# Kernel optimization log

Hardware: AMD Instinct MI355X
Metric: run time of the kernel (lower is better)

Reference implementation:

```python
import jax, jax.numpy as jnp
import numpy as np

B, H, W, C = 1, 180, 360, 192
WS, SHIFT, NH = 6, 3, 6
MLAT, MLON = H // WS, W // WS
NW = MLAT * MLON
N = WS * WS
HD = C // NH
SCALE = HD ** -0.5
EPS = 1e-5


def _rel_index():
    # earth-specific relative position index: (MLAT, N, N) int32
    ch = np.arange(WS)
    cw = np.arange(WS)
    coords = np.stack(np.meshgrid(ch, cw, indexing='ij')).reshape(2, -1)  # (2, N)
    rel = coords[:, :, None] - coords[:, None, :]                         # (2, N, N)
    idx = (rel[0] + WS - 1) * (2 * WS - 1) + (rel[1] + WS - 1)            # (N, N)
    off = np.arange(MLAT) * (2 * WS - 1) * (2 * WS - 1)                   # per-latitude offset
    return (idx[None, :, :] + off[:, None, None]).astype(np.int32)


def _attn_mask():
    # standard shifted-window mask: (NW, N, N), 0 or -100
    img = np.zeros((H, W), dtype=np.int32)
    cnt = 0
    for hs in (slice(0, -WS), slice(-WS, -SHIFT), slice(-SHIFT, None)):
        for ws_ in (slice(0, -WS), slice(-WS, -SHIFT), slice(-SHIFT, None)):
            img[hs, ws_] = cnt
            cnt += 1
    wins = img.reshape(MLAT, WS, MLON, WS).transpose(0, 2, 1, 3).reshape(NW, N)
    diff = wins[:, None, :] - wins[:, :, None]
    return np.where(diff != 0, -100.0, 0.0).astype(np.float32)

_RPI = jnp.asarray(_rel_index())     # (MLAT, N, N)
_MASK = jnp.asarray(_attn_mask())    # (NW, N, N)


def _layernorm(x, g, b):
    mu = jnp.mean(x, axis=-1, keepdims=True)
    var = jnp.mean(jnp.square(x - mu), axis=-1, keepdims=True)
    return (x - mu) * jax.lax.rsqrt(var + EPS) * g + b


def _window_partition(x):
    # (B, H, W, C) -> (B*NW, N, C)
    x = x.reshape(B, MLAT, WS, MLON, WS, C).transpose(0, 1, 3, 2, 4, 5)
    return x.reshape(B * NW, N, C)


def _window_reverse(w):
    # (B*NW, N, C) -> (B, H, W, C)
    x = w.reshape(B, MLAT, MLON, WS, WS, C).transpose(0, 1, 3, 2, 4, 5)
    return x.reshape(B, H, W, C)


def setup_inputs() -> dict:
    key = jax.random.key(0)
    ks = jax.random.split(key, 6)
    s = 0.02
    return {
        'x': jax.random.normal(ks[0], (B, H * W, C), jnp.float32),
        'norm1_w': jnp.ones((C,), jnp.float32),
        'norm1_b': jnp.zeros((C,), jnp.float32),
        'qkv_w': jax.random.normal(ks[1], (C, 3 * C), jnp.float32) * s,
        'qkv_b': jnp.zeros((3 * C,), jnp.float32),
        'proj_w': jax.random.normal(ks[2], (C, C), jnp.float32) * s,
        'proj_b': jnp.zeros((C,), jnp.float32),
        'bias_table': jax.random.normal(ks[3], (MLAT * (2 * WS - 1) ** 2, NH), jnp.float32) * s,
        'norm2_w': jnp.ones((C,), jnp.float32),
        'norm2_b': jnp.zeros((C,), jnp.float32),
        'fc1_w': jax.random.normal(ks[4], (C, 4 * C), jnp.float32) * s,
        'fc1_b': jnp.zeros((4 * C,), jnp.float32),
        'fc2_w': jax.random.normal(ks[5], (4 * C, C), jnp.float32) * s,
        'fc2_b': jnp.zeros((C,), jnp.float32),
    }


def reference(x, norm1_w, norm1_b, qkv_w, qkv_b, proj_w, proj_b, bias_table,
              norm2_w, norm2_b, fc1_w, fc1_b, fc2_w, fc2_b):
    shortcut = x
    h = _layernorm(x, norm1_w, norm1_b).reshape(B, H, W, C)
    # cyclic shift
    h = jnp.roll(h, shift=(-SHIFT, -SHIFT), axis=(1, 2))
    xw = _window_partition(h)                                   # (B*NW, N, C)

    qkv = xw @ qkv_w + qkv_b                                    # (B_, N, 3C)
    qkv = qkv.reshape(B * NW, N, 3, NH, HD).transpose(2, 0, 3, 1, 4)
    q, k, v = qkv[0], qkv[1], qkv[2]                            # (B_, NH, N, HD)

    # earth-specific relative position bias, gathered per latitude row
    bias = jnp.take(bias_table, _RPI, axis=0)                   # (MLAT, N, N, NH)
    bias = bias.transpose(0, 3, 1, 2)[:, None]                  # (MLAT, 1, NH, N, N)
    bias = jnp.broadcast_to(bias, (MLAT, MLON, NH, N, N)).reshape(NW, NH, N, N)
    bias = bias + _MASK[:, None]                                # add shift mask

    attn = jnp.einsum('bhnd,bhmd->bhnm', q, k) * SCALE + bias
    attn = jax.nn.softmax(attn, axis=-1)
    av = jnp.einsum('bhnm,bhmd->bhnd', attn, v)                 # (B_, NH, N, HD)
    av = av.transpose(0, 2, 1, 3).reshape(B * NW, N, C)
    av = av @ proj_w + proj_b

    h = _window_reverse(av)
    h = jnp.roll(h, shift=(SHIFT, SHIFT), axis=(1, 2)).reshape(B, H * W, C)
    x = shortcut + h

    m = _layernorm(x, norm2_w, norm2_b)
    m = jax.nn.gelu(m @ fc1_w + fc1_b, approximate=False) @ fc2_w + fc2_b
    return x + m
```

## Files before the change

kernel.cpp:

```cpp
#include <hip/hip_runtime.h>
#include <hip/hip_bf16.h>

constexpr int HH   = 180;
constexpr int WW   = 360;
constexpr int CC   = 192;
constexpr int WS   = 6;
constexpr int SHIFT= 3;
constexpr int NH   = 6;
constexpr int MLAT = HH / WS;
constexpr int MLON = WW / WS;
constexpr int NWIN = MLAT * MLON;
constexpr int NTOK = WS * WS;
constexpr int HD   = CC / NH;
constexpr long M_TOK = (long)NWIN * NTOK;
constexpr long M_PAD = 65024;
constexpr float SCALE_F = 0.17677669529663687f;

typedef unsigned short ushort_t;
using bf16x8 = __attribute__((ext_vector_type(8))) short;
using f32x4  = __attribute__((ext_vector_type(4))) float;

static __device__ inline float b2f(ushort_t u) {
    union { float f; unsigned int i; } v; v.i = ((unsigned int)u) << 16; return v.f;
}
static __device__ inline ushort_t f2b(float f) {
    __hip_bfloat16 h = __float2bfloat16(f);
    return *(ushort_t*)&h;
}
static __device__ inline unsigned int cvtpk(float lo, float hi) {
    unsigned int r;
    asm("v_cvt_pk_bf16_f32 %0, %1, %2" : "=v"(r) : "v"(lo), "v"(hi));
    return r;
}

static __device__ inline void gload_lds16(const ushort_t* g, ushort_t* l) {
    __builtin_amdgcn_global_load_lds(
        (const __attribute__((address_space(1))) unsigned int*)g,
        (__attribute__((address_space(3))) unsigned int*)l, 16, 0, 0);
}

static __device__ inline int win_map(int ti) {
    int w = ti / NTOK, n = ti - w * NTOK;
    int mlat = w / MLON, mlon = w - mlat * MLON;
    int sh = mlat * WS + n / WS, sw = mlon * WS + (n % WS);
    int hh = sh + SHIFT; if (hh >= HH) hh -= HH;
    int ww2 = sw + SHIFT; if (ww2 >= WW) ww2 -= WW;
    return hh * WW + ww2;
}

__global__ void transpose_all(const float* __restrict__ qkv_w, const float* __restrict__ proj_w,
                              const float* __restrict__ fc1_w, const float* __restrict__ fc2_w,
                              ushort_t* __restrict__ wqkv, ushort_t* __restrict__ wproj,
                              ushort_t* __restrict__ wfc1, ushort_t* __restrict__ wfc2) {
    int e = blockIdx.x * 256 + threadIdx.x;
    const float* in; ushort_t* out; int K, N;
    if (e < 110592)      { in = qkv_w;  out = wqkv;  K = 192; N = 576; }
    else if (e < 147456) { e -= 110592; in = proj_w; out = wproj; K = 192; N = 192; }
    else if (e < 294912) { e -= 147456; in = fc1_w;  out = wfc1;  K = 192; N = 768; }
    else if (e < 442368) { e -= 294912; in = fc2_w;  out = wfc2;  K = 768; N = 192; }
    else return;
    int n = e / K, k = e - n * K;
    out[e] = f2b(in[(long)k * N + n]);
}

__global__ void zero_bf16(ushort_t* __restrict__ p, int count) {
    int e = blockIdx.x * 256 + threadIdx.x;
    if (e < count) p[e] = 0;
}

static __device__ inline int region1d(int p, int L) {
    return (p < L - WS) ? 0 : ((p < L - SHIFT) ? 1 : 2);
}

__global__ void bias_mask_precompute(const float* __restrict__ bt, float* __restrict__ bm) {
    int idx = blockIdx.x * 256 + threadIdx.x;
    if (idx >= MLAT * 2 * NH * 36 * 48) return;
    int e = idx;
    int j = e % 48; e /= 48;
    int i = e % 36; e /= 36;
    int h = e % NH; e /= NH;
    int lt = e % 2;
    int mlat = e / 2;
    if (j >= 36) { bm[idx] = -1e30f; return; }
    int ih = i / WS, iw = i - ih * WS;
    int jh = j / WS, jw = j - jh * WS;
    int bidx = mlat * 121 + (ih - jh + 5) * 11 + (iw - jw + 5);
    float v = bt[bidx * NH + h];
    int mlon = lt ? (MLON - 1) : 0;
    int ri = region1d(mlat * WS + ih, HH) * 3 + region1d(mlon * WS + iw, WW);
    int rj = region1d(mlat * WS + jh, HH) * 3 + region1d(mlon * WS + jw, WW);
    if (ri != rj) v += -100.0f;
    bm[idx] = v;
}

__global__ __launch_bounds__(256) void ln1_window_kernel(
    const float* __restrict__ x, const float* __restrict__ g, const float* __restrict__ b,
    ushort_t* __restrict__ xw)
{
    long t = (long)blockIdx.x * 4 + (threadIdx.x >> 6);
    int lane = threadIdx.x & 63;
    if (t >= M_PAD) return;
    if (t >= M_TOK) {
        ushort_t* o = xw + t * CC;
        o[lane] = 0; o[lane + 64] = 0; o[lane + 128] = 0;
        return;
    }
    int pp = win_map((int)t);
    const float* row = x + (long)pp * CC;
    float v0 = row[lane], v1 = row[lane + 64], v2 = row[lane + 128];
    float s = v0 + v1 + v2;
    float ss = v0 * v0 + v1 * v1 + v2 * v2;
    #pragma unroll
    for (int o = 32; o > 0; o >>= 1) { s += __shfl_xor(s, o, 64); ss += __shfl_xor(ss, o, 64); }
    float mu = s * (1.0f / CC);
    float var = ss * (1.0f / CC) - mu * mu;
    float rinv = rsqrtf(var + 1e-5f);
    ushort_t* o = xw + t * CC;
    o[lane]       = f2b((v0 - mu) * rinv * g[lane]       + b[lane]);
    o[lane + 64]  = f2b((v1 - mu) * rinv * g[lane + 64]  + b[lane + 64]);
    o[lane + 128] = f2b((v2 - mu) * rinv * g[lane + 128] + b[lane + 128]);
}

#define BM 128
#define BN 192
#define BK 64

template<int MODE, int KK>
__global__ __launch_bounds__(512, 4) void gemm_bf16(
    const ushort_t* __restrict__ A, const ushort_t* __restrict__ Bt,
    const float* __restrict__ bias,
    ushort_t* __restrict__ outb, float* __restrict__ outf,
    const float* __restrict__ resid,
    const float* __restrict__ g2, const float* __restrict__ b2,
    int N, long Mguard, int ncol, int nwg)
{
    constexpr int nt = KK / BK;
    __shared__ __align__(16) ushort_t lds[40960];

    int tid = threadIdx.x;
    int lane = tid & 63;
    int wid = tid >> 6;
    int lr = lane & 15, lg = lane >> 4;
    int wm = wid >> 2, wn = wid & 3;

    int orig = blockIdx.x;
    int q = nwg >> 3, r8 = nwg & 7;
    int xcd = orig & 7, pos = orig >> 3;
    int wg = (xcd < r8 ? xcd * (q + 1) : r8 * (q + 1) + (xcd - r8) * q) + pos;
    int brow = wg / ncol, bcol = wg - brow * ncol;
    long bm0 = (long)brow * BM;
    int n0 = bcol * BN;

#define STAGE(b, k0) do { \
    char* base = (char*)lds + (b) * 40960; \
    _Pragma("unroll") \
    for (int i = 0; i < 5; ++i) { \
        int abs_b = tid * 16 + i * 8192; \
        int isA = abs_b < 16384; \
        int loc = isA ? abs_b : abs_b - 16384; \
        int row = loc >> 7, cb = loc & 127; \
        int scol = (cb ^ ((row & 7) << 4)) >> 1; \
        const ushort_t* src = isA ? &A[(bm0 + row) * KK + (k0) + scol] \
                                  : &Bt[(long)(n0 + row) * KK + (k0) + scol]; \
        gload_lds16(src, (ushort_t*)(base + abs_b)); \
    } \
} while (0)

    f32x4 acc[4][3] = {};

    STAGE(0, 0);
    asm volatile("s_waitcnt vmcnt(0)" ::: "memory");
    __builtin_amdgcn_s_barrier();

    int xr = (lr & 7) << 4;

    #pragma unroll
    for (int kt = 0; kt < nt; ++kt) {
        if (kt + 1 < nt) {
            STAGE((kt + 1) & 1, (kt + 1) * BK);
            asm volatile("s_waitcnt vmcnt(5)" ::: "memory");
        } else {
            asm volatile("s_waitcnt vmcnt(0)" ::: "memory");
        }
        __builtin_amdgcn_s_barrier();

        const char* base = (const char*)lds + (kt & 1) * 40960;
        __builtin_amdgcn_s_setprio(1);
        #pragma unroll
        for (int s = 0; s < 2; ++s) {
            bf16x8 af[4], bfr[3];
            #pragma unroll
            for (int fm = 0; fm < 4; ++fm) {
                int row = wm * 64 + fm * 16 + lr;
                af[fm] = *(const bf16x8*)(base + row * 128 + ((s * 64 + lg * 16) ^ xr));
            }
            #pragma unroll
            for (int fn = 0; fn < 3; ++fn) {
                int row = wn * 48 + fn * 16 + lr;
                bfr[fn] = *(const bf16x8*)(base + 16384 + row * 128 + ((s * 64 + lg * 16) ^ xr));
            }
            #pragma unroll
            for (int fm = 0; fm < 4; ++fm)
                #pragma unroll
                for (int fn = 0; fn < 3; ++fn)
                    acc[fm][fn] = __builtin_amdgcn_mfma_f32_16x16x32_bf16(af[fm], bfr[fn], acc[fm][fn], 0, 0, 0);
        }
        __builtin_amdgcn_s_setprio(0);
        asm volatile("s_waitcnt lgkmcnt(0)" ::: "memory");
        __builtin_amdgcn_s_barrier();
    }
#undef STAGE

    float bv[3];
    #pragma unroll
    for (int fn = 0; fn < 3; ++fn) bv[fn] = bias[n0 + wn * 48 + fn * 16 + lr];

    if (MODE == 0 || MODE == 1) {
        ushort_t* bb = lds + wid * 896;
        #pragma unroll
        for (int fm = 0; fm < 4; ++fm) {
            #pragma unroll
            for (int fn = 0; fn < 3; ++fn) {
                #pragma unroll
                for (int r = 0; r < 4; ++r) {
                    float v = acc[fm][fn][r] + bv[fn];
                    if (MODE == 0) {
                        if (n0 == 0) v *= SCALE_F;
                    }
                    if (MODE == 1) {
                        float e2 = exp2f(v * -2.4556617f);
                        v = v * __builtin_amdgcn_rcpf(1.0f + e2);
                    }
                    bb[(lg * 4 + r) * 56 + fn * 16 + lr] = f2b(v);
                }
            }
            #pragma unroll
            for (int i = 0; i < 2; ++i) {
                int cid = i * 64 + lane;
                if (cid < 96) {
                    int row = cid / 6, c6 = cid - row * 6;
                    uint4 val = *(const uint4*)&bb[row * 56 + c6 * 8];
                    long grow = bm0 + wm * 64 + fm * 16 + row;
                    *(uint4*)&outb[grow * (long)N + n0 + wn * 48 + c6 * 8] = val;
                }
            }
        }
    } else if (MODE == 3) {
        float* fb = (float*)lds + wid * 832;
        #pragma unroll
        for (int fm = 0; fm < 4; ++fm) {
            #pragma unroll
            for (int fn = 0; fn < 3; ++fn)
                #pragma unroll
                for (int r = 0; r < 4; ++r)
                    fb[(lg * 4 + r) * 52 + fn * 16 + lr] = acc[fm][fn][r] + bv[fn];
            #pragma unroll
            for (int i = 0; i < 3; ++i) {
                int cid = i * 64 + lane;
                int row = cid / 12, c4 = cid - row * 12;
                f32x4 val = *(const f32x4*)&fb[row * 52 + c4 * 4];
                long grow = bm0 + wm * 64 + fm * 16 + row;
                int col = wn * 48 + c4 * 4;
                if (grow < Mguard) {
                    float* p = &outf[grow * 192 + col];
                    f32x4 old = *(const f32x4*)p;
                    *(f32x4*)p = old + val;
                }
            }
        }
    } else {
        float* redS = (float*)((char*)lds + 73728);
        float* redQ = (float*)((char*)lds + 75776);
        int*   row_map = (int*)((char*)lds + 78336);
        if (tid < BM) {
            long t = bm0 + tid;
            row_map[tid] = (t < M_TOK) ? win_map((int)t) : -1;
        }
        asm volatile("s_waitcnt lgkmcnt(0)" ::: "memory");
        __builtin_amdgcn_s_barrier();

        #pragma unroll
        for (int fm = 0; fm < 4; ++fm) {
            float s4[4], q4[4];
            #pragma unroll
            for (int r = 0; r < 4; ++r) {
                int lrow = wm * 64 + fm * 16 + lg * 4 + r;
                int pp = row_map[lrow];
                float s = 0.f, qq = 0.f;
                #pragma unroll
                for (int fn = 0; fn < 3; ++fn) {
                    float vv = acc[fm][fn][r] + bv[fn];
                    if (pp >= 0) vv += resid[(long)pp * 192 + wn * 48 + fn * 16 + lr];
                    acc[fm][fn][r] = vv;
                    s += vv; qq += vv * vv;
                }
                s4[r] = s; q4[r] = qq;
            }
            #pragma unroll
            for (int off = 1; off < 16; off <<= 1)
                #pragma unroll
                for (int r = 0; r < 4; ++r) {
                    s4[r] += __shfl_xor(s4[r], off, 64);
                    q4[r] += __shfl_xor(q4[r], off, 64);
                }
            if (lr == 0) {
                #pragma unroll
                for (int r = 0; r < 4; ++r) {
                    int row = wm * 64 + fm * 16 + lg * 4 + r;
                    redS[row * 4 + wn] = s4[r];
                    redQ[row * 4 + wn] = q4[r];
                }
            }
        }
        asm volatile("s_waitcnt lgkmcnt(0)" ::: "memory");
        __builtin_amdgcn_s_barrier();

        float gv[3], bv2[3];
        #pragma unroll
        for (int fn = 0; fn < 3; ++fn) {
            gv[fn]  = g2[wn * 48 + fn * 16 + lr];
            bv2[fn] = b2[wn * 48 + fn * 16 + lr];
        }

        float* fb = (float*)lds + wid * 832;
        ushort_t* bb = (ushort_t*)((char*)lds + 32768) + wid * 896;
        #pragma unroll
        for (int fm = 0; fm < 4; ++fm) {
            float mu4[4], rin4[4];
            #pragma unroll
            for (int r = 0; r < 4; ++r) {
                int row = wm * 64 + fm * 16 + lg * 4 + r;
                float s = redS[row * 4 + 0] + redS[row * 4 + 1] + redS[row * 4 + 2] + redS[row * 4 + 3];
                float qq = redQ[row * 4 + 0] + redQ[row * 4 + 1] + redQ[row * 4 + 2] + redQ[row * 4 + 3];
                float mu = s * (1.0f / 192.0f);
                float var = qq * (1.0f / 192.0f) - mu * mu;
                mu4[r] = mu;
                rin4[r] = rsqrtf(var + 1e-5f);
            }
            #pragma unroll
            for (int fn = 0; fn < 3; ++fn)
                #pragma unroll
                for (int r = 0; r < 4; ++r) {
                    float vv = acc[fm][fn][r];
                    fb[(lg * 4 + r) * 52 + fn * 16 + lr] = vv;
                    bb[(lg * 4 + r) * 56 + fn * 16 + lr] =
                        f2b((vv - mu4[r]) * rin4[r] * gv[fn] + bv2[fn]);
                }
            #pragma unroll
            for (int i = 0; i < 3; ++i) {
                int cid = i * 64 + lane;
                int row = cid / 12, c4 = cid - row * 12;
                int pp = row_map[wm * 64 + fm * 16 + row];
                if (pp >= 0) {
                    f32x4 val = *(const f32x4*)&fb[row * 52 + c4 * 4];
                    *(f32x4*)&outf[(long)pp * 192 + wn * 48 + c4 * 4] = val;
                }
            }
            #pragma unroll
            for (int i = 0; i < 2; ++i) {
                int cid = i * 64 + lane;
                if (cid < 96) {
                    int row = cid / 6, c6 = cid - row * 6;
                    int pp = row_map[wm * 64 + fm * 16 + row];
                    if (pp >= 0) {
                        uint4 val = *(const uint4*)&bb[row * 56 + c6 * 8];
                        *(uint4*)&outb[(long)pp * 192 + wn * 48 + c6 * 8] = val;
                    }
                }
            }
        }
    }
}

__global__ __launch_bounds__(256) void attn_mfma_kernel(
    const ushort_t* __restrict__ qkv,
    const float* __restrict__ bm,
    ushort_t* __restrict__ av)
{
    int wid = threadIdx.x >> 6, lane = threadIdx.x & 63;
    int unit = blockIdx.x * 4 + wid;
    int w = unit / NH, h = unit - (unit / NH) * NH;
    int mlat = w / MLON, mlon = w - mlat * MLON;
    int lr = lane & 15, lg = lane >> 4;

    const ushort_t* Qb = qkv + (long)w * NTOK * 576 + h * HD;
    const ushort_t* Kb = Qb + 192;
    const ushort_t* Vb = Qb + 384;

    bf16x8 kf[3], qf[3];
    #pragma unroll
    for (int t = 0; t < 3; ++t) {
        kf[t] = *(const bf16x8*)&Kb[(long)(t * 16 + lr) * 576 + 8 * lg];
        qf[t] = *(const bf16x8*)&Qb[(long)(t * 16 + lr) * 576 + 8 * lg];
    }
    f32x4 st[3][3] = {};
    #pragma unroll
    for (int mt = 0; mt < 3; ++mt)
        #pragma unroll
        for (int qt = 0; qt < 3; ++qt)
            st[mt][qt] = __builtin_amdgcn_mfma_f32_16x16x32_bf16(kf[mt], qf[qt], st[mt][qt], 0, 0, 0);

    bf16x8 vf[2][2];
    #pragma unroll
    for (int nd = 0; nd < 2; ++nd)
        #pragma unroll
        for (int kt = 0; kt < 2; ++kt)
            #pragma unroll
            for (int j = 0; j < 8; ++j)
                ((short*)&vf[nd][kt])[j] =
                    (short)Vb[(long)(kt * 32 + 8 * lg + j) * 576 + nd * 16 + lr];

    const float* bb = bm + (((mlat * 2 + (mlon == MLON - 1)) * NH) + h) * (36 * 48);

    f32x4 o[2][3] = {};
    int src0 = ((2 * (lg & 1)) << 4) | lr;
    int src1 = src0 + 16;

    #pragma unroll
    for (int qt = 0; qt < 3; ++qt) {
        int qrow = qt * 16 + lr;
        int qq = qrow < 36 ? qrow : 35;
        float v[3][4];
        #pragma unroll
        for (int mt = 0; mt < 3; ++mt) {
            f32x4 b4 = *(const f32x4*)&bb[qq * 48 + mt * 16 + 4 * lg];
            #pragma unroll
            for (int r = 0; r < 4; ++r) v[mt][r] = st[mt][qt][r] + b4[r];
        }
        float mx = v[0][0];
        #pragma unroll
        for (int mt = 0; mt < 3; ++mt)
            #pragma unroll
            for (int r = 0; r < 4; ++r) mx = fmaxf(mx, v[mt][r]);
        mx = fmaxf(mx, __shfl_xor(mx, 16, 64));
        mx = fmaxf(mx, __shfl_xor(mx, 32, 64));
        float p[3][4], sum = 0.f;
        #pragma unroll
        for (int mt = 0; mt < 3; ++mt)
            #pragma unroll
            for (int r = 0; r < 4; ++r) { p[mt][r] = __expf(v[mt][r] - mx); sum += p[mt][r]; }
        sum += __shfl_xor(sum, 16, 64);
        sum += __shfl_xor(sum, 32, 64);
        float rs = 1.0f / sum;

        unsigned int pk[3][2];
        #pragma unroll
        for (int mt = 0; mt < 3; ++mt) {
            pk[mt][0] = cvtpk(p[mt][0] * rs, p[mt][1] * rs);
            pk[mt][1] = cvtpk(p[mt][2] * rs, p[mt][3] * rs);
        }
        unsigned int f0[4], f1[4];
        {
            unsigned int a, b;
            a = (unsigned)__shfl((int)pk[0][0], src0, 64); b = (unsigned)__shfl((int)pk[1][0], src0, 64);
            f0[0] = (lg < 2) ? a : b;
            a = (unsigned)__shfl((int)pk[0][1], src0, 64); b = (unsigned)__shfl((int)pk[1][1], src0, 64);
            f0[1] = (lg < 2) ? a : b;
            a = (unsigned)__shfl((int)pk[0][0], src1, 64); b = (unsigned)__shfl((int)pk[1][0], src1, 64);
            f0[2] = (lg < 2) ? a : b;
            a = (unsigned)__shfl((int)pk[0][1], src1, 64); b = (unsigned)__shfl((int)pk[1][1], src1, 64);
            f0[3] = (lg < 2) ? a : b;
            f1[0] = (lg < 2) ? (unsigned)__shfl((int)pk[2][0], src0, 64) : 0u;
            f1[1] = (lg < 2) ? (unsigned)__shfl((int)pk[2][1], src0, 64) : 0u;
            f1[2] = (lg < 2) ? (unsigned)__shfl((int)pk[2][0], src1, 64) : 0u;
            f1[3] = (lg < 2) ? (unsigned)__shfl((int)pk[2][1], src1, 64) : 0u;
        }
        union { unsigned int u[4]; bf16x8 v8; } pf0, pf1;
        pf0.u[0] = f0[0]; pf0.u[1] = f0[1]; pf0.u[2] = f0[2]; pf0.u[3] = f0[3];
        pf1.u[0] = f1[0]; pf1.u[1] = f1[1]; pf1.u[2] = f1[2]; pf1.u[3] = f1[3];

        #pragma unroll
        for (int nd = 0; nd < 2; ++nd) {
            o[nd][qt] = __builtin_amdgcn_mfma_f32_16x16x32_bf16(vf[nd][0], pf0.v8, o[nd][qt], 0, 0, 0);
            o[nd][qt] = __builtin_amdgcn_mfma_f32_16x16x32_bf16(vf[nd][1], pf1.v8, o[nd][qt], 0, 0, 0);
        }
    }

    #pragma unroll
    for (int qt = 0; qt < 3; ++qt) {
        int qrow = qt * 16 + lr;
        if (qrow < NTOK) {
            #pragma unroll
            for (int nd = 0; nd < 2; ++nd) {
                uint2 pkd;
                pkd.x = cvtpk(o[nd][qt][0], o[nd][qt][1]);
                pkd.y = cvtpk(o[nd][qt][2], o[nd][qt][3]);
                *(uint2*)&av[((long)w * NTOK + qrow) * CC + h * HD + nd * 16 + 4 * lg] = pkd;
            }
        }
    }
}

extern "C" void kernel_launch(void* const* d_in, const int* in_sizes, int n_in,
                              void* d_out, int out_size, void* d_ws, size_t ws_size,
                              hipStream_t stream) {
    const float* x        = (const float*)d_in[0];
    const float* n1w      = (const float*)d_in[1];
    const float* n1b      = (const float*)d_in[2];
    const float* qkv_w    = (const float*)d_in[3];
    const float* qkv_b    = (const float*)d_in[4];
    const float* proj_w   = (const float*)d_in[5];
    const float* proj_b   = (const float*)d_in[6];
    const float* btab     = (const float*)d_in[7];
    const float* n2w      = (const float*)d_in[8];
    const float* n2b      = (const float*)d_in[9];
    const float* fc1_w    = (const float*)d_in[10];
    const float* fc1_b    = (const float*)d_in[11];
    const float* fc2_w    = (const float*)d_in[12];
    const float* fc2_b    = (const float*)d_in[13];
    float* out = (float*)d_out;

    char* p = (char*)d_ws;
    ushort_t* xw  = (ushort_t*)p;  p += M_PAD * 192 * 2;
    ushort_t* big = (ushort_t*)p;  p += M_PAD * 768 * 2;
    ushort_t* av  = (ushort_t*)p;  p += M_PAD * 192 * 2;
    ushort_t* wqkv = (ushort_t*)p; p += 576 * 192 * 2;
    ushort_t* wproj= (ushort_t*)p; p += 192 * 192 * 2;
    ushort_t* wfc1 = (ushort_t*)p; p += 768 * 192 * 2;
    ushort_t* wfc2 = (ushort_t*)p; p += 192 * 768 * 2;
    float*    bmask= (float*)p;    p += MLAT * 2 * NH * 36 * 48 * 4;

    transpose_all<<<(442368 + 255)/256, 256, 0, stream>>>(
        qkv_w, proj_w, fc1_w, fc2_w, wqkv, wproj, wfc1, wfc2);
    bias_mask_precompute<<<(MLAT*2*NH*36*48 + 255)/256, 256, 0, stream>>>(btab, bmask);
    zero_bf16<<<((int)(M_PAD - M_TOK)*192 + 255)/256, 256, 0, stream>>>(av + M_TOK * 192, (int)(M_PAD - M_TOK) * 192);

    ln1_window_kernel<<<M_PAD / 4, 256, 0, stream>>>(x, n1w, n1b, xw);

    gemm_bf16<0, 192><<<508 * 3, 512, 0, stream>>>(
        xw, wqkv, qkv_b, big, nullptr, nullptr, nullptr, nullptr, 576, M_PAD, 3, 508 * 3);

    attn_mfma_kernel<<<NWIN * NH / 4, 256, 0, stream>>>(big, bmask, av);

    gemm_bf16<2, 192><<<508, 512, 0, stream>>>(
        av, wproj, proj_b, xw, out, x, n2w, n2b, 192, M_TOK, 1, 508);

    gemm_bf16<1, 192><<<508 * 4, 512, 0, stream>>>(
        xw, wfc1, fc1_b, big, nullptr, nullptr, nullptr, nullptr, 768, M_PAD, 4, 508 * 4);

    gemm_bf16<3, 768><<<508, 512, 0, stream>>>(
        big, wfc2, fc2_b, nullptr, out, nullptr, nullptr, nullptr, 192, M_TOK, 1, 508);
}
```

Baseline: 193.9 us.

## Single-buffer GEMM LDS, raise occupancy, per-warp full-row tiles for fused LayerNorm epilogue

Removes double buffering in the bf16 GEMM so LDS drops to 40 KB, and raises the occupancy hint for the non-LN modes. For the residual+LayerNorm mode, each warp now owns 16 full rows (1x12 fragments), so row statistics are reduced with intra-warp shuffles instead of a cross-warp LDS reduction and barrier. The epilogue writes in column chunks through a smaller per-warp staging area. The cost is that global loads no longer overlap with MFMA compute, since each k-step stages then waits on vmcnt(0), and the LN mode uses more accumulator registers per lane.

```diff
diff --git a/kernel.cpp b/kernel.cpp
--- a/kernel.cpp
+++ b/kernel.cpp
@@ -126,7 +126,7 @@
 #define BK 64
 
 template<int MODE, int KK>
-__global__ __launch_bounds__(512, 4) void gemm_bf16(
+__global__ __launch_bounds__(512, (MODE == 2 ? 4 : 6)) void gemm_bf16(
     const ushort_t* __restrict__ A, const ushort_t* __restrict__ Bt,
     const float* __restrict__ bias,
     ushort_t* __restrict__ outb, float* __restrict__ outf,
@@ -135,13 +135,16 @@
     int N, long Mguard, int ncol, int nwg)
 {
     constexpr int nt = KK / BK;
-    __shared__ __align__(16) ushort_t lds[40960];
+    constexpr int WMT = (MODE == 2) ? 1 : 4;
+    constexpr int WNT = (MODE == 2) ? 12 : 3;
+    __shared__ __align__(16) ushort_t lds[20480];
 
     int tid = threadIdx.x;
     int lane = tid & 63;
     int wid = tid >> 6;
     int lr = lane & 15, lg = lane >> 4;
-    int wm = wid >> 2, wn = wid & 3;
+    int wrow0 = (MODE == 2) ? wid * 16 : (wid >> 2) * 64;
+    int wcol0 = (MODE == 2) ? 0 : (wid & 3) * 48;
 
     int orig = blockIdx.x;
     int q = nwg >> 3, r8 = nwg & 7;
@@ -151,8 +154,7 @@
     long bm0 = (long)brow * BM;
     int n0 = bcol * BN;
 
-#define STAGE(b, k0) do { \
-    char* base = (char*)lds + (b) * 40960; \
+#define STAGE(k0) do { \
     _Pragma("unroll") \
     for (int i = 0; i < 5; ++i) { \
         int abs_b = tid * 16 + i * 8192; \
@@ -162,47 +164,37 @@
         int scol = (cb ^ ((row & 7) << 4)) >> 1; \
         const ushort_t* src = isA ? &A[(bm0 + row) * KK + (k0) + scol] \
                                   : &Bt[(long)(n0 + row) * KK + (k0) + scol]; \
-        gload_lds16(src, (ushort_t*)(base + abs_b)); \
+        gload_lds16(src, (ushort_t*)((char*)lds + abs_b)); \
     } \
 } while (0)
 
-    f32x4 acc[4][3] = {};
-
-    STAGE(0, 0);
-    asm volatile("s_waitcnt vmcnt(0)" ::: "memory");
-    __builtin_amdgcn_s_barrier();
-
+    f32x4 acc[WMT][WNT] = {};
     int xr = (lr & 7) << 4;
 
     #pragma unroll
     for (int kt = 0; kt < nt; ++kt) {
-        if (kt + 1 < nt) {
-            STAGE((kt + 1) & 1, (kt + 1) * BK);
-            asm volatile("s_waitcnt vmcnt(5)" ::: "memory");
-        } else {
-            asm volatile("s_waitcnt vmcnt(0)" ::: "memory");
-        }
+        STAGE(kt * BK);
+        asm volatile("s_waitcnt vmcnt(0)" ::: "memory");
         __builtin_amdgcn_s_barrier();
 
-        const char* base = (const char*)lds + (kt & 1) * 40960;
         __builtin_amdgcn_s_setprio(1);
         #pragma unroll
         for (int s = 0; s < 2; ++s) {
-            bf16x8 af[4], bfr[3];
-            #pragma unroll
-            for (int fm = 0; fm < 4; ++fm) {
-                int row = wm * 64 + fm * 16 + lr;
-                af[fm] = *(const bf16x8*)(base + row * 128 + ((s * 64 + lg * 16) ^ xr));
-            }
-            #pragma unroll
-            for (int fn = 0; fn < 3; ++fn) {
-                int row = wn * 48 + fn * 16 + lr;
-                bfr[fn] = *(const bf16x8*)(base + 16384 + row * 128 + ((s * 64 + lg * 16) ^ xr));
-            }
-            #pragma unroll
-            for (int fm = 0; fm < 4; ++fm)
+            bf16x8 af[WMT], bfr[WNT];
+            #pragma unroll
+            for (int fm = 0; fm < WMT; ++fm) {
+                int row = wrow0 + fm * 16 + lr;
+                af[fm] = *(const bf16x8*)((const char*)lds + row * 128 + ((s * 64 + lg * 16) ^ xr));
+            }
+            #pragma unroll
+            for (int fn = 0; fn < WNT; ++fn) {
+                int row = wcol0 + fn * 16 + lr;
+                bfr[fn] = *(const bf16x8*)((const char*)lds + 16384 + row * 128 + ((s * 64 + lg * 16) ^ xr));
+            }
+            #pragma unroll
+            for (int fm = 0; fm < WMT; ++fm)
                 #pragma unroll
-                for (int fn = 0; fn < 3; ++fn)
+                for (int fn = 0; fn < WNT; ++fn)
                     acc[fm][fn] = __builtin_amdgcn_mfma_f32_16x16x32_bf16(af[fm], bfr[fn], acc[fm][fn], 0, 0, 0);
         }
         __builtin_amdgcn_s_setprio(0);
@@ -211,11 +203,10 @@
     }
 #undef STAGE
 
-    float bv[3];
-    #pragma unroll
-    for (int fn = 0; fn < 3; ++fn) bv[fn] = bias[n0 + wn * 48 + fn * 16 + lr];
-
     if (MODE == 0 || MODE == 1) {
+        float bv[3];
+        #pragma unroll
+        for (int fn = 0; fn < 3; ++fn) bv[fn] = bias[n0 + wcol0 + fn * 16 + lr];
         ushort_t* bb = lds + wid * 896;
         #pragma unroll
         for (int fm = 0; fm < 4; ++fm) {
@@ -240,12 +231,15 @@
                 if (cid < 96) {
                     int row = cid / 6, c6 = cid - row * 6;
                     uint4 val = *(const uint4*)&bb[row * 56 + c6 * 8];
-                    long grow = bm0 + wm * 64 + fm * 16 + row;
-                    *(uint4*)&outb[grow * (long)N + n0 + wn * 48 + c6 * 8] = val;
+                    long grow = bm0 + wrow0 + fm * 16 + row;
+                    *(uint4*)&outb[grow * (long)N + n0 + wcol0 + c6 * 8] = val;
                 }
             }
         }
     } else if (MODE == 3) {
+        float bv[3];
+        #pragma unroll
+        for (int fn = 0; fn < 3; ++fn) bv[fn] = bias[n0 + wcol0 + fn * 16 + lr];
         float* fb = (float*)lds + wid * 832;
         #pragma unroll
         for (int fm = 0; fm < 4; ++fm) {
@@ -259,8 +253,8 @@
                 int cid = i * 64 + lane;
                 int row = cid / 12, c4 = cid - row * 12;
                 f32x4 val = *(const f32x4*)&fb[row * 52 + c4 * 4];
-                long grow = bm0 + wm * 64 + fm * 16 + row;
-                int col = wn * 48 + c4 * 4;
+                long grow = bm0 + wrow0 + fm * 16 + row;
+                int col = wcol0 + c4 * 4;
                 if (grow < Mguard) {
                     float* p = &outf[grow * 192 + col];
                     f32x4 old = *(const f32x4*)p;
@@ -269,9 +263,7 @@
             }
         }
     } else {
-        float* redS = (float*)((char*)lds + 73728);
-        float* redQ = (float*)((char*)lds + 75776);
-        int*   row_map = (int*)((char*)lds + 78336);
+        int* row_map = (int*)((char*)lds + 36864);
         if (tid < BM) {
             long t = bm0 + tid;
             row_map[tid] = (t < M_TOK) ? win_map((int)t) : -1;
@@ -279,93 +271,80 @@
         asm volatile("s_waitcnt lgkmcnt(0)" ::: "memory");
         __builtin_amdgcn_s_barrier();
 
-        #pragma unroll
-        for (int fm = 0; fm < 4; ++fm) {
-            float s4[4], q4[4];
-            #pragma unroll
-            for (int r = 0; r < 4; ++r) {
-                int lrow = wm * 64 + fm * 16 + lg * 4 + r;
-                int pp = row_map[lrow];
-                float s = 0.f, qq = 0.f;
+        float bvv[12];
+        #pragma unroll
+        for (int fn = 0; fn < 12; ++fn) bvv[fn] = bias[fn * 16 + lr];
+
+        float mu4[4], rin4[4];
+        #pragma unroll
+        for (int r = 0; r < 4; ++r) {
+            int lrow = wid * 16 + lg * 4 + r;
+            int pp = row_map[lrow];
+            float s = 0.f, qq = 0.f;
+            #pragma unroll
+            for (int fn = 0; fn < 12; ++fn) {
+                float vv = acc[0][fn][r] + bvv[fn];
+                if (pp >= 0) vv += resid[(long)pp * 192 + fn * 16 + lr];
+                acc[0][fn][r] = vv;
+                s += vv; qq += vv * vv;
+            }
+            #pragma unroll
+            for (int off = 1; off < 16; off <<= 1) {
+                s += __shfl_xor(s, off, 64);
+                qq += __shfl_xor(qq, off, 64);
+            }
+            float mu = s * (1.0f / 192.0f);
+            float var = qq * (1.0f / 192.0f) - mu * mu;
+            mu4[r] = mu;
+            rin4[r] = rsqrtf(var + 1e-5f);
+        }
+
+        float gv[12], bv2[12];
+        #pragma unroll
+        for (int fn = 0; fn < 12; ++fn) {
+            gv[fn]  = g2[fn * 16 + lr];
+            bv2[fn] = b2[fn * 16 + lr];
+        }
+
+        char* ws = (char*)lds + wid * 4608;
+        #pragma unroll
+        for (int c = 0; c < 3; ++c) {
+            float* fbc = (float*)ws;
+            #pragma unroll
+            for (int fn2 = 0; fn2 < 4; ++fn2) {
+                int fn = c * 4 + fn2;
                 #pragma unroll
-                for (int fn = 0; fn < 3; ++fn) {
-                    float vv = acc[fm][fn][r] + bv[fn];
-                    if (pp >= 0) vv += resid[(long)pp * 192 + wn * 48 + fn * 16 + lr];
-                    acc[fm][fn][r] = vv;
-                    s += vv; qq += vv * vv;
+                for (int r = 0; r < 4; ++r)
+                    fbc[(lg * 4 + r) * 68 + fn2 * 16 + lr] = acc[0][fn][r];
+            }
+            #pragma unroll
+            for (int i = 0; i < 4; ++i) {
+                int cid = i * 64 + lane;
+                int row = cid >> 4, c4 = cid & 15;
+                int pp = row_map[wid * 16 + row];
+                if (pp >= 0) {
+                    f32x4 val = *(const f32x4*)&fbc[row * 68 + c4 * 4];
+                    *(f32x4*)&outf[(long)pp * 192 + c * 64 + c4 * 4] = val;
                 }
-                s4[r] = s; q4[r] = qq;
-            }
-            #pragma unroll
-            for (int off = 1; off < 16; off <<= 1)
+            }
+            ushort_t* bbc = (ushort_t*)ws;
+            #pragma unroll
+            for (int fn2 = 0; fn2 < 4; ++fn2) {
+                int fn = c * 4 + fn2;
                 #pragma unroll
                 for (int r = 0; r < 4; ++r) {
-                    s4[r] += __shfl_xor(s4[r], off, 64);
-                    q4[r] += __shfl_xor(q4[r], off, 64);
-                }
-            if (lr == 0) {
-                #pragma unroll
-                for (int r = 0; r < 4; ++r) {
-                    int row = wm * 64 + fm * 16 + lg * 4 + r;
-                    redS[row * 4 + wn] = s4[r];
-                    redQ[row * 4 + wn] = q4[r];
-                }
-            }
-        }
-        asm volatile("s_waitcnt lgkmcnt(0)" ::: "memory");
-        __builtin_amdgcn_s_barrier();
-
-        float gv[3], bv2[3];
-        #pragma unroll
-        for (int fn = 0; fn < 3; ++fn) {
-            gv[fn]  = g2[wn * 48 + fn * 16 + lr];
-            bv2[fn] = b2[wn * 48 + fn * 16 + lr];
-        }
-
-        float* fb = (float*)lds + wid * 832;
-        ushort_t* bb = (ushort_t*)((char*)lds + 32768) + wid * 896;
-        #pragma unroll
-        for (int fm = 0; fm < 4; ++fm) {
-            float mu4[4], rin4[4];
-            #pragma unroll
-            for (int r = 0; r < 4; ++r) {
-                int row = wm * 64 + fm * 16 + lg * 4 + r;
-                float s = redS[row * 4 + 0] + redS[row * 4 + 1] + redS[row * 4 + 2] + redS[row * 4 + 3];
-                float qq = redQ[row * 4 + 0] + redQ[row * 4 + 1] + redQ[row * 4 + 2] + redQ[row * 4 + 3];
-                float mu = s * (1.0f / 192.0f);
-                float var = qq * (1.0f / 192.0f) - mu * mu;
-                mu4[r] = mu;
-                rin4[r] = rsqrtf(var + 1e-5f);
-            }
-            #pragma unroll
-            for (int fn = 0; fn < 3; ++fn)
-                #pragma unroll
-                for (int r = 0; r < 4; ++r) {
-                    float vv = acc[fm][fn][r];
-                    fb[(lg * 4 + r) * 52 + fn * 16 + lr] = vv;
-                    bb[(lg * 4 + r) * 56 + fn * 16 + lr] =
-                        f2b((vv - mu4[r]) * rin4[r] * gv[fn] + bv2[fn]);
-                }
-            #pragma unroll
-            for (int i = 0; i < 3; ++i) {
-                int cid = i * 64 + lane;
-                int row = cid / 12, c4 = cid - row * 12;
-                int pp = row_map[wm * 64 + fm * 16 + row];
-                if (pp >= 0) {
-                    f32x4 val = *(const f32x4*)&fb[row * 52 + c4 * 4];
-                    *(f32x4*)&outf[(long)pp * 192 + wn * 48 + c4 * 4] = val;
+                    float v = (acc[0][fn][r] - mu4[r]) * rin4[r] * gv[fn] + bv2[fn];
+                    bbc[(lg * 4 + r) * 72 + fn2 * 16 + lr] = f2b(v);
                 }
             }
             #pragma unroll
             for (int i = 0; i < 2; ++i) {
                 int cid = i * 64 + lane;
-                if (cid < 96) {
-                    int row = cid / 6, c6 = cid - row * 6;
-                    int pp = row_map[wm * 64 + fm * 16 + row];
-                    if (pp >= 0) {
-                        uint4 val = *(const uint4*)&bb[row * 56 + c6 * 8];
-                        *(uint4*)&outb[(long)pp * 192 + wn * 48 + c6 * 8] = val;
-                    }
+                int row = cid >> 3, c8 = cid & 7;
+                int pp = row_map[wid * 16 + row];
+                if (pp >= 0) {
+                    uint4 val = *(const uint4*)&bbc[row * 72 + c8 * 8];
+                    *(uint4*)&outb[(long)pp * 192 + c * 64 + c8 * 8] = val;
                 }
             }
         }
```

New measurement: 329.2 us. 69.8% more time.

## Fuse MLP fc1, GELU and fc2 into one kernel keeping hidden in LDS

Applied to the files above, without the earlier changes.

Replaces the separate fc1 GEMM (writing a 768-wide bf16 hidden activation to global memory) and fc2 GEMM with a single kernel. Each 128-row tile computes fc1 in 128-column chunks, applies the GELU approximation, stores the chunk in LDS, and immediately accumulates it into the fc2 output. This removes the global write and re-read of the hidden tensor and one launch. In exchange, fc1 loads are not pipelined, there are many barriers, and only 508 workgroups run, which may limit occupancy.

```diff
diff --git a/kernel.cpp b/kernel.cpp
--- a/kernel.cpp
+++ b/kernel.cpp
@@ -215,7 +215,7 @@
     #pragma unroll
     for (int fn = 0; fn < 3; ++fn) bv[fn] = bias[n0 + wn * 48 + fn * 16 + lr];
 
-    if (MODE == 0 || MODE == 1) {
+    if (MODE == 0) {
         ushort_t* bb = lds + wid * 896;
         #pragma unroll
         for (int fm = 0; fm < 4; ++fm) {
@@ -224,13 +224,7 @@
                 #pragma unroll
                 for (int r = 0; r < 4; ++r) {
                     float v = acc[fm][fn][r] + bv[fn];
-                    if (MODE == 0) {
-                        if (n0 == 0) v *= SCALE_F;
-                    }
-                    if (MODE == 1) {
-                        float e2 = exp2f(v * -2.4556617f);
-                        v = v * __builtin_amdgcn_rcpf(1.0f + e2);
-                    }
+                    if (n0 == 0) v *= SCALE_F;
                     bb[(lg * 4 + r) * 56 + fn * 16 + lr] = f2b(v);
                 }
             }
@@ -242,29 +236,6 @@
                     uint4 val = *(const uint4*)&bb[row * 56 + c6 * 8];
                     long grow = bm0 + wm * 64 + fm * 16 + row;
                     *(uint4*)&outb[grow * (long)N + n0 + wn * 48 + c6 * 8] = val;
-                }
-            }
-        }
-    } else if (MODE == 3) {
-        float* fb = (float*)lds + wid * 832;
-        #pragma unroll
-        for (int fm = 0; fm < 4; ++fm) {
-            #pragma unroll
-            for (int fn = 0; fn < 3; ++fn)
-                #pragma unroll
-                for (int r = 0; r < 4; ++r)
-                    fb[(lg * 4 + r) * 52 + fn * 16 + lr] = acc[fm][fn][r] + bv[fn];
-            #pragma unroll
-            for (int i = 0; i < 3; ++i) {
-                int cid = i * 64 + lane;
-                int row = cid / 12, c4 = cid - row * 12;
-                f32x4 val = *(const f32x4*)&fb[row * 52 + c4 * 4];
-                long grow = bm0 + wm * 64 + fm * 16 + row;
-                int col = wn * 48 + c4 * 4;
-                if (grow < Mguard) {
-                    float* p = &outf[grow * 192 + col];
-                    f32x4 old = *(const f32x4*)p;
-                    *(f32x4*)p = old + val;
                 }
             }
         }
@@ -367,6 +338,168 @@
                         *(uint4*)&outb[(long)pp * 192 + wn * 48 + c6 * 8] = val;
                     }
                 }
+            }
+        }
+    }
+}
+
+__global__ __launch_bounds__(512, 4) void fused_mlp(
+    const ushort_t* __restrict__ xw, const ushort_t* __restrict__ w1,
+    const float* __restrict__ b1, const ushort_t* __restrict__ w2,
+    const float* __restrict__ b2v, float* __restrict__ outf, int nwg)
+{
+    __shared__ __align__(16) ushort_t lds[33792];
+    int tid = threadIdx.x;
+    int lane = tid & 63;
+    int wid = tid >> 6;
+    int lr = lane & 15, lg = lane >> 4;
+    int wm = wid >> 2;
+    int wc2 = wid & 3;
+
+    int orig = blockIdx.x;
+    int q = nwg >> 3, r8 = nwg & 7;
+    int xcd = orig & 7, pos = orig >> 3;
+    int wg = (xcd < r8 ? xcd * (q + 1) : r8 * (q + 1) + (xcd - r8) * q) + pos;
+    long bm0 = (long)wg * 128;
+
+    int xr = (lr & 7) << 4;
+    char* R1 = (char*)lds;
+    char* Hb = (char*)lds + 32768;
+    ushort_t* Hu = (ushort_t*)Hb;
+
+#define STAGE_W2(sub) do { \
+    _Pragma("unroll") \
+    for (int i = 0; i < 3; ++i) { \
+        int abs_b = tid * 16 + i * 8192; \
+        int row = abs_b >> 7, cb = abs_b & 127; \
+        int scol = (cb ^ ((row & 7) << 4)) >> 1; \
+        gload_lds16(&w2[(long)row * 768 + ch * 128 + (sub) * 64 + scol], \
+                    (ushort_t*)(R1 + abs_b)); \
+    } \
+} while (0)
+
+#define C_COMPUTE(sub) do { \
+    __builtin_amdgcn_s_setprio(1); \
+    _Pragma("unroll") \
+    for (int s = 0; s < 2; ++s) { \
+        bf16x8 af2[4], bf2[3]; \
+        _Pragma("unroll") \
+        for (int fm = 0; fm < 4; ++fm) { \
+            int row = wm * 64 + fm * 16 + lr; \
+            af2[fm] = *(const bf16x8*)(Hb + row * 272 + (sub) * 128 + s * 64 + lg * 16); \
+        } \
+        _Pragma("unroll") \
+        for (int fn = 0; fn < 3; ++fn) { \
+            int row = wc2 * 48 + fn * 16 + lr; \
+            bf2[fn] = *(const bf16x8*)(R1 + row * 128 + ((s * 64 + lg * 16) ^ xr)); \
+        } \
+        _Pragma("unroll") \
+        for (int fm = 0; fm < 4; ++fm) \
+            _Pragma("unroll") \
+            for (int fn = 0; fn < 3; ++fn) \
+                acc2[fm][fn] = __builtin_amdgcn_mfma_f32_16x16x32_bf16(af2[fm], bf2[fn], acc2[fm][fn], 0, 0, 0); \
+    } \
+    __builtin_amdgcn_s_setprio(0); \
+} while (0)
+
+    f32x4 acc2[4][3] = {};
+
+    #pragma unroll 1
+    for (int ch = 0; ch < 6; ++ch) {
+        f32x4 acc1[4][2] = {};
+        #pragma unroll
+        for (int kt = 0; kt < 3; ++kt) {
+            #pragma unroll
+            for (int i = 0; i < 4; ++i) {
+                int abs_b = tid * 16 + i * 8192;
+                int isA = abs_b < 16384;
+                int loc = isA ? abs_b : abs_b - 16384;
+                int row = loc >> 7, cb = loc & 127;
+                int scol = (cb ^ ((row & 7) << 4)) >> 1;
+                const ushort_t* src = isA ? &xw[(bm0 + row) * 192 + kt * 64 + scol]
+                                          : &w1[(long)(ch * 128 + row) * 192 + kt * 64 + scol];
+                gload_lds16(src, (ushort_t*)(R1 + abs_b));
+            }
+            asm volatile("s_waitcnt vmcnt(0)" ::: "memory");
+            __builtin_amdgcn_s_barrier();
+            __builtin_amdgcn_s_setprio(1);
+            #pragma unroll
+            for (int s = 0; s < 2; ++s) {
+                bf16x8 af[4], bf1[2];
+                #pragma unroll
+                for (int fm = 0; fm < 4; ++fm) {
+                    int row = wm * 64 + fm * 16 + lr;
+                    af[fm] = *(const bf16x8*)(R1 + row * 128 + ((s * 64 + lg * 16) ^ xr));
+                }
+                #pragma unroll
+                for (int fn = 0; fn < 2; ++fn) {
+                    int row = wc2 * 32 + fn * 16 + lr;
+                    bf1[fn] = *(const bf16x8*)(R1 + 16384 + row * 128 + ((s * 64 + lg * 16) ^ xr));
+                }
+                #pragma unroll
+                for (int fm = 0; fm < 4; ++fm)
+                    #pragma unroll
+                    for (int fn = 0; fn < 2; ++fn)
+                        acc1[fm][fn] = __builtin_amdgcn_mfma_f32_16x16x32_bf16(af[fm], bf1[fn], acc1[fm][fn], 0, 0, 0);
+            }
+            __builtin_amdgcn_s_setprio(0);
+            asm volatile("s_waitcnt lgkmcnt(0)" ::: "memory");
+            __builtin_amdgcn_s_barrier();
+        }
+
+        STAGE_W2(0);
+
+        float bv1a = b1[ch * 128 + wc2 * 32 + lr];
+        float bv1b = b1[ch * 128 + wc2 * 32 + 16 + lr];
+        #pragma unroll
+        for (int fm = 0; fm < 4; ++fm)
+            #pragma unroll
+            for (int fn = 0; fn < 2; ++fn)
+                #pragma unroll
+                for (int r = 0; r < 4; ++r) {
+                    float v = acc1[fm][fn][r] + (fn ? bv1b : bv1a);
+                    float e2 = exp2f(v * -2.4556617f);
+                    v = v * __builtin_amdgcn_rcpf(1.0f + e2);
+                    Hu[(wm * 64 + fm * 16 + lg * 4 + r) * 136 + wc2 * 32 + fn * 16 + lr] = f2b(v);
+                }
+        asm volatile("s_waitcnt vmcnt(0) lgkmcnt(0)" ::: "memory");
+        __builtin_amdgcn_s_barrier();
+
+        C_COMPUTE(0);
+        asm volatile("s_waitcnt lgkmcnt(0)" ::: "memory");
+        __builtin_amdgcn_s_barrier();
+        STAGE_W2(1);
+        asm volatile("s_waitcnt vmcnt(0)" ::: "memory");
+        __builtin_amdgcn_s_barrier();
+        C_COMPUTE(1);
+        asm volatile("s_waitcnt lgkmcnt(0)" ::: "memory");
+        __builtin_amdgcn_s_barrier();
+    }
+#undef STAGE_W2
+#undef C_COMPUTE
+
+    float bv2[3];
+    #pragma unroll
+    for (int fn = 0; fn < 3; ++fn) bv2[fn] = b2v[wc2 * 48 + fn * 16 + lr];
+    float* fb = (float*)R1 + wid * 832;
+    #pragma unroll
+    for (int fm = 0; fm < 4; ++fm) {
+        #pragma unroll
+        for (int fn = 0; fn < 3; ++fn)
+            #pragma unroll
+            for (int r = 0; r < 4; ++r)
+                fb[(lg * 4 + r) * 52 + fn * 16 + lr] = acc2[fm][fn][r] + bv2[fn];
+        #pragma unroll
+        for (int i = 0; i < 3; ++i) {
+            int cid = i * 64 + lane;
+            int row = cid / 12, c4 = cid - row * 12;
+            f32x4 val = *(const f32x4*)&fb[row * 52 + c4 * 4];
+            long grow = bm0 + wm * 64 + fm * 16 + row;
+            int col = wc2 * 48 + c4 * 4;
+            if (grow < M_TOK) {
+                float* p = &outf[grow * 192 + col];
+                f32x4 old = *(const f32x4*)p;
+                *(f32x4*)p = old + val;
             }
         }
     }
@@ -535,9 +668,5 @@
     gemm_bf16<2, 192><<<508, 512, 0, stream>>>(
         av, wproj, proj_b, xw, out, x, n2w, n2b, 192, M_TOK, 1, 508);
 
-    gemm_bf16<1, 192><<<508 * 4, 512, 0, stream>>>(
-        xw, wfc1, fc1_b, big, nullptr, nullptr, nullptr, nullptr, 768, M_PAD, 4, 508 * 4);
-
-    gemm_bf16<3, 768><<<508, 512, 0, stream>>>(
-        big, wfc2, fc2_b, nullptr, out, nullptr, nullptr, nullptr, 192, M_TOK, 1, 508);
-}
+    fused_mlp<<<508, 512, 0, stream>>>(xw, wfc1, fc1_b, wfc2, fc2_b, out, 508);
+}
```

Result: slower. 232.1 us (+19.7%).
